# Kernel tuning notes

Measured on AMD Instinct MI355X. Metric: run time of the kernel, lower is better.

## Reference

```python
import jax, jax.numpy as jnp
import numpy as np

D_MODEL = 2048
N_HEADS = 16
HEAD_DIM = D_MODEL // N_HEADS
CLIP_QKV = 6.0
LN_EPS = 1e-5


def _layernorm(x, g, b):
    mu = jnp.mean(x, axis=-1, keepdims=True)
    var = jnp.mean(jnp.square(x - mu), axis=-1, keepdims=True)
    return (x - mu) * jax.lax.rsqrt(var + LN_EPS) * g + b


def setup_inputs() -> dict:
    key = jax.random.key(0)
    ks = jax.random.split(key, 8)
    B, S = 2, 2048
    x = jax.random.normal(ks[0], (B, S, D_MODEL), dtype=jnp.float32)
    attn_bias = jax.random.normal(ks[1], (1, N_HEADS, 1, S), dtype=jnp.float32)
    key_padding_mask = jnp.ones((B, S), dtype=bool)
    Wqkv_w = jax.random.normal(ks[2], (3 * D_MODEL, D_MODEL), dtype=jnp.float32) * 0.02
    Wqkv_b = jnp.zeros((3 * D_MODEL,), dtype=jnp.float32)
    q_ln_g = jnp.ones((D_MODEL,), dtype=jnp.float32)
    q_ln_b = jnp.zeros((D_MODEL,), dtype=jnp.float32)
    k_ln_g = jnp.ones((D_MODEL,), dtype=jnp.float32)
    k_ln_b = jnp.zeros((D_MODEL,), dtype=jnp.float32)
    out_w = jax.random.normal(ks[3], (D_MODEL, D_MODEL), dtype=jnp.float32) * 0.02
    out_b = jnp.zeros((D_MODEL,), dtype=jnp.float32)
    return {
        'x': x, 'attn_bias': attn_bias, 'key_padding_mask': key_padding_mask,
        'Wqkv_w': Wqkv_w, 'Wqkv_b': Wqkv_b,
        'q_ln_g': q_ln_g, 'q_ln_b': q_ln_b, 'k_ln_g': k_ln_g, 'k_ln_b': k_ln_b,
        'out_w': out_w, 'out_b': out_b,
    }


def reference(x, attn_bias, key_padding_mask, Wqkv_w, Wqkv_b,
              q_ln_g, q_ln_b, k_ln_g, k_ln_b, out_w, out_b):
    B, S, _ = x.shape
    # Fused QKV projection + clip
    qkv = jnp.einsum('bsd,ed->bse', x, Wqkv_w) + Wqkv_b
    qkv = jnp.clip(qkv, -CLIP_QKV, CLIP_QKV)
    q, k, v = jnp.split(qkv, 3, axis=-1)
    # QK LayerNorm over full d_model
    q = _layernorm(q, q_ln_g, q_ln_b)
    k = _layernorm(k, k_ln_g, k_ln_b)
    # [b, s, d_model] -> [b, h, s, head_dim]
    q = q.reshape(B, S, N_HEADS, HEAD_DIM).transpose(0, 2, 1, 3)
    k = k.reshape(B, S, N_HEADS, HEAD_DIM).transpose(0, 2, 1, 3)
    v = v.reshape(B, S, N_HEADS, HEAD_DIM).transpose(0, 2, 1, 3)
    scale = 1.0 / np.sqrt(HEAD_DIM).astype(np.float32)
    scores = jnp.einsum('bhqd,bhkd->bhqk', q, k) * scale  # [b, h, s, s]
    scores = scores + attn_bias
    neg_inf = jnp.array(-jnp.inf, dtype=scores.dtype)
    scores = jnp.where(key_padding_mask[:, None, None, :], scores, neg_inf)
    causal = jnp.tril(jnp.ones((S, S), dtype=bool))
    scores = jnp.where(causal[None, None, :, :], scores, neg_inf)
    probs = jax.nn.softmax(scores, axis=-1)
    ctx = jnp.einsum('bhqk,bhkd->bhqd', probs, v)
    ctx = ctx.transpose(0, 2, 1, 3).reshape(B, S, D_MODEL)
    out = jnp.einsum('bsd,ed->bse', ctx, out_w) + out_b
    return out
```

## Files before the change

kernel.cpp:

```cpp
#include <hip/hip_runtime.h>

typedef unsigned short u16;
typedef unsigned int u32;
typedef __bf16 bf16x8 __attribute__((ext_vector_type(8)));
typedef float f32x4 __attribute__((ext_vector_type(4)));

#define DEV static __device__ __forceinline__

constexpr int D_MODEL = 2048;
constexpr int N_HEADS = 16;
constexpr int HEAD_DIM = 128;
constexpr int BB = 2;
constexpr int S = 2048;
constexpr int NTOK = BB * S;
constexpr int E3 = 3 * D_MODEL;
constexpr float CLIP_QKV = 6.0f;
constexpr float LN_EPS = 1e-5f;
constexpr float NEG_BIG = -30000.0f;

DEV u16 f2bf(float f) {
    u32 u = __float_as_uint(f);
    u = (u + 0x7FFFu + ((u >> 16) & 1u)) >> 16;
    return (u16)u;
}
DEV float bf2f(u16 h) { return __uint_as_float(((u32)h) << 16); }

DEV void stage8_f32(const float* __restrict__ src, u16* __restrict__ dst) {
    const float4 f0 = *reinterpret_cast<const float4*>(src);
    const float4 f1 = *reinterpret_cast<const float4*>(src + 4);
    u16 h[8] = {f2bf(f0.x), f2bf(f0.y), f2bf(f0.z), f2bf(f0.w),
                f2bf(f1.x), f2bf(f1.y), f2bf(f1.z), f2bf(f1.w)};
    *reinterpret_cast<uint4*>(dst) = *reinterpret_cast<const uint4*>(h);
}

DEV void gload16(const u16* g, u16* l) {
    __builtin_amdgcn_global_load_lds(
        (const __attribute__((address_space(1))) void*)g,
        (__attribute__((address_space(3))) void*)l, 16, 0, 0);
}

__global__ __launch_bounds__(256)
void k_cvt(const float* __restrict__ s, u16* __restrict__ d, int n8) {
    const int i = blockIdx.x * 256 + threadIdx.x;
    if (i < n8) stage8_f32(s + (size_t)i * 8, d + (size_t)i * 8);
}

template<bool DO_CLIP, bool OUT32>
__global__ __launch_bounds__(256)
void k_gemm_bt(const u16* __restrict__ A, const u16* __restrict__ Bm,
               const float* __restrict__ bias, void* __restrict__ Cp,
               int M, int N, int K) {
    __shared__ __align__(16) u16 As[128 * 32];
    __shared__ __align__(16) u16 Bs[128 * 32];

    const int tid = threadIdx.x;
    const int lane = tid & 63, w = tid >> 6;
    const int quad = lane >> 4, l16 = lane & 15;
    const int wm = w >> 1, wn = w & 1;
    const int m0 = blockIdx.y * 128, n0 = blockIdx.x * 128;

    f32x4 acc[4][4] = {};

    for (int k0 = 0; k0 < K; k0 += 32) {
        __syncthreads();
        #pragma unroll
        for (int j = 0; j < 2; ++j) {
            const int c = w * 128 + j * 64 + lane;
            const int row = c >> 2, cc = c & 3;
            gload16(A  + (size_t)(m0 + row) * K + k0 + cc * 8, &As[c * 8]);
            gload16(Bm + (size_t)(n0 + row) * K + k0 + cc * 8, &Bs[c * 8]);
        }
        __syncthreads();

        bf16x8 af[4], bfv[4];
        #pragma unroll
        for (int mt = 0; mt < 4; ++mt)
            af[mt] = *reinterpret_cast<const bf16x8*>(&As[(wm * 64 + mt * 16 + l16) * 32 + quad * 8]);
        #pragma unroll
        for (int nt = 0; nt < 4; ++nt)
            bfv[nt] = *reinterpret_cast<const bf16x8*>(&Bs[(wn * 64 + nt * 16 + l16) * 32 + quad * 8]);
        #pragma unroll
        for (int mt = 0; mt < 4; ++mt)
            #pragma unroll
            for (int nt = 0; nt < 4; ++nt)
                acc[mt][nt] = __builtin_amdgcn_mfma_f32_16x16x32_bf16(af[mt], bfv[nt], acc[mt][nt], 0, 0, 0);
    }

    #pragma unroll
    for (int mt = 0; mt < 4; ++mt) {
        const int row = m0 + wm * 64 + mt * 16 + quad * 4;
        #pragma unroll
        for (int nt = 0; nt < 4; ++nt) {
            const int col = n0 + wn * 64 + nt * 16 + l16;
            const float bv = bias[col];
            #pragma unroll
            for (int r = 0; r < 4; ++r) {
                float v = acc[mt][nt][r] + bv;
                if (DO_CLIP) v = fminf(CLIP_QKV, fmaxf(-CLIP_QKV, v));
                if (OUT32)
                    ((float*)Cp)[(size_t)(row + r) * N + col] = v;
                else
                    ((u16*)Cp)[(size_t)(row + r) * N + col] = f2bf(v);
            }
        }
    }
}

__global__ __launch_bounds__(256)
void k_ln(const u16* __restrict__ qkvb,
          const float* __restrict__ gq, const float* __restrict__ bq,
          const float* __restrict__ gk, const float* __restrict__ bk,
          u16* __restrict__ qh, u16* __restrict__ kh) {
    __shared__ float red[8];
    const int tok = blockIdx.x;
    const int b = tok >> 11, s = tok & (S - 1);
    const int tid = threadIdx.x, lane = tid & 63, w = tid >> 6;

    #pragma unroll
    for (int part = 0; part < 2; ++part) {
        const int c0 = tid * 8;
        const u16* src = qkvb + (size_t)tok * E3 + part * D_MODEL + c0;
        u16 hx[8];
        *reinterpret_cast<uint4*>(hx) = *reinterpret_cast<const uint4*>(src);
        float x[8], sum = 0.f, sq = 0.f;
        #pragma unroll
        for (int j = 0; j < 8; ++j) { x[j] = bf2f(hx[j]); sum += x[j]; sq += x[j] * x[j]; }
        #pragma unroll
        for (int off = 1; off < 64; off <<= 1) {
            sum += __shfl_xor(sum, off, 64);
            sq  += __shfl_xor(sq,  off, 64);
        }
        __syncthreads();
        if (lane == 0) { red[w] = sum; red[4 + w] = sq; }
        __syncthreads();
        sum = red[0] + red[1] + red[2] + red[3];
        sq  = red[4] + red[5] + red[6] + red[7];
        const float mean = sum * (1.0f / D_MODEL);
        const float var  = fmaxf(sq * (1.0f / D_MODEL) - mean * mean, 0.0f);
        const float rstd = rsqrtf(var + LN_EPS);
        const float* g  = part ? gk : gq;
        const float* be = part ? bk : bq;
        u16 o[8];
        #pragma unroll
        for (int j = 0; j < 8; ++j)
            o[j] = f2bf((x[j] - mean) * rstd * g[c0 + j] + be[c0 + j]);
        const int h = c0 >> 7, d = c0 & (HEAD_DIM - 1);
        u16* dst = (part ? kh : qh) + ((size_t)((b * N_HEADS + h) * S + s)) * HEAD_DIM + d;
        *reinterpret_cast<uint4*>(dst) = *reinterpret_cast<uint4*>(o);
    }
}

__global__ __launch_bounds__(256)
void k_vtrans(const u16* __restrict__ qkvb, u16* __restrict__ vt) {
    constexpr int LDT = 136;
    __shared__ __align__(16) u16 tile[64 * LDT];
    const int blk = blockIdx.x;
    const int st = blk & 31, h = (blk >> 5) & 15, b = blk >> 9;
    const int s0 = st * 64;
    const int tid = threadIdx.x;

    #pragma unroll
    for (int i = 0; i < 4; ++i) {
        const int chunk = tid + i * 256;
        const int row = chunk >> 4, c8 = (chunk & 15) * 8;
        const u16* src = qkvb + (size_t)(b * S + s0 + row) * E3 + 2 * D_MODEL + h * HEAD_DIM + c8;
        *reinterpret_cast<uint4*>(&tile[row * LDT + c8]) = *reinterpret_cast<const uint4*>(src);
    }
    __syncthreads();
    #pragma unroll
    for (int i = 0; i < 4; ++i) {
        const int chunk = tid + i * 256;
        const int d = chunk >> 3, s8 = (chunk & 7) * 8;
        u16 o[8];
        #pragma unroll
        for (int j = 0; j < 8; ++j) o[j] = tile[(s8 + j) * LDT + d];
        u16* dst = vt + ((size_t)(b * N_HEADS + h) * HEAD_DIM + d) * S + s0 + s8;
        *reinterpret_cast<uint4*>(dst) = *reinterpret_cast<uint4*>(o);
    }
}

__global__ __launch_bounds__(256)
void k_attn(const u16* __restrict__ qh, const u16* __restrict__ kh,
            const u16* __restrict__ vt, const float* __restrict__ bias,
            u16* __restrict__ ctx) {
    constexpr int BQ = 128, BKV = 64;
    constexpr int LDK = 136;
    constexpr int LDV = 72;
    constexpr int LDP = 72;
    __shared__ __align__(16) u16 Ks[64 * LDK];
    __shared__ __align__(16) u16 Vs[128 * LDV];
    __shared__ __align__(16) u16 Ps[128 * LDP];

    const int blk = blockIdx.x;
    const int bh = blk & 31;
    const int qi = 15 - (blk >> 5);
    const int b = bh >> 4, h = bh & 15;
    const int q0 = qi * BQ;

    const int tid = threadIdx.x, lane = tid & 63, w = tid >> 6;
    const int quad = lane >> 4, l16 = lane & 15;

    const size_t bhS = (size_t)(b * N_HEADS + h) * S;
    const u16* Qt = qh + (bhS + q0) * HEAD_DIM;
    const u16* Kt = kh + bhS * HEAD_DIM;
    const u16* Vt = vt + (size_t)(b * N_HEADS + h) * HEAD_DIM * S;

    bf16x8 aq[2][4];
    #pragma unroll
    for (int mt = 0; mt < 2; ++mt)
        #pragma unroll
        for (int ks = 0; ks < 4; ++ks)
            aq[mt][ks] = *reinterpret_cast<const bf16x8*>(
                Qt + (size_t)(w * 32 + mt * 16 + l16) * HEAD_DIM + ks * 32 + quad * 8);

    f32x4 o[2][8] = {};
    float m_i[2][4], l_i[2][4];
    #pragma unroll
    for (int mt = 0; mt < 2; ++mt)
        #pragma unroll
        for (int r = 0; r < 4; ++r) { m_i[mt][r] = NEG_BIG; l_i[mt][r] = 0.f; }

    const float scale = 0.08838834764831845f;
    const int nkv = 2 * (qi + 1);

    for (int t = 0; t < nkv; ++t) {
        const int k0 = t * BKV;
        __syncthreads();
        #pragma unroll
        for (int i = 0; i < 4; ++i) {
            const int chunk = tid + i * 256;
            const int key = chunk >> 4, c8 = (chunk & 15) * 8;
            *reinterpret_cast<uint4*>(&Ks[key * LDK + c8]) =
                *reinterpret_cast<const uint4*>(Kt + (size_t)(k0 + key) * HEAD_DIM + c8);
        }
        #pragma unroll
        for (int i = 0; i < 4; ++i) {
            const int chunk = tid + i * 256;
            const int d = chunk >> 3, s8 = (chunk & 7) * 8;
            *reinterpret_cast<uint4*>(&Vs[d * LDV + s8]) =
                *reinterpret_cast<const uint4*>(Vt + (size_t)d * S + k0 + s8);
        }
        __syncthreads();

        f32x4 sc[2][4] = {};
        #pragma unroll
        for (int ks = 0; ks < 4; ++ks) {
            bf16x8 bk[4];
            #pragma unroll
            for (int nt = 0; nt < 4; ++nt)
                bk[nt] = *reinterpret_cast<const bf16x8*>(&Ks[(nt * 16 + l16) * LDK + ks * 32 + quad * 8]);
            #pragma unroll
            for (int mt = 0; mt < 2; ++mt)
                #pragma unroll
                for (int nt = 0; nt < 4; ++nt)
                    sc[mt][nt] = __builtin_amdgcn_mfma_f32_16x16x32_bf16(aq[mt][ks], bk[nt], sc[mt][nt], 0, 0, 0);
        }

        float bv[4];
        #pragma unroll
        for (int nt = 0; nt < 4; ++nt) bv[nt] = bias[h * S + k0 + nt * 16 + l16];
        const bool need_mask = (t >= 2 * qi);
        #pragma unroll
        for (int mt = 0; mt < 2; ++mt)
            #pragma unroll
            for (int nt = 0; nt < 4; ++nt) {
                const int kpos = k0 + nt * 16 + l16;
                #pragma unroll
                for (int r = 0; r < 4; ++r) {
                    float v = sc[mt][nt][r] * scale + bv[nt];
                    if (need_mask) {
                        const int qpos = q0 + w * 32 + mt * 16 + quad * 4 + r;
                        if (kpos > qpos) v = NEG_BIG;
                    }
                    sc[mt][nt][r] = v;
                }
            }

        #pragma unroll
        for (int mt = 0; mt < 2; ++mt)
            #pragma unroll
            for (int r = 0; r < 4; ++r) {
                float mx = fmaxf(fmaxf(sc[mt][0][r], sc[mt][1][r]), fmaxf(sc[mt][2][r], sc[mt][3][r]));
                mx = fmaxf(mx, __shfl_xor(mx, 1, 64));
                mx = fmaxf(mx, __shfl_xor(mx, 2, 64));
                mx = fmaxf(mx, __shfl_xor(mx, 4, 64));
                mx = fmaxf(mx, __shfl_xor(mx, 8, 64));
                const float mnew = fmaxf(m_i[mt][r], mx);
                const float alpha = __expf(m_i[mt][r] - mnew);
                float rs = 0.f;
                #pragma unroll
                for (int nt = 0; nt < 4; ++nt) {
                    const float p = __expf(sc[mt][nt][r] - mnew);
                    sc[mt][nt][r] = p;
                    rs += p;
                }
                rs += __shfl_xor(rs, 1, 64);
                rs += __shfl_xor(rs, 2, 64);
                rs += __shfl_xor(rs, 4, 64);
                rs += __shfl_xor(rs, 8, 64);
                l_i[mt][r] = l_i[mt][r] * alpha + rs;
                m_i[mt][r] = mnew;
                #pragma unroll
                for (int nt = 0; nt < 8; ++nt) o[mt][nt][r] *= alpha;
            }

        #pragma unroll
        for (int mt = 0; mt < 2; ++mt)
            #pragma unroll
            for (int nt = 0; nt < 4; ++nt)
                #pragma unroll
                for (int r = 0; r < 4; ++r)
                    Ps[(w * 32 + mt * 16 + quad * 4 + r) * LDP + nt * 16 + l16] = f2bf(sc[mt][nt][r]);

        __syncthreads();

        #pragma unroll
        for (int ks = 0; ks < 2; ++ks) {
            bf16x8 ap[2];
            #pragma unroll
            for (int mt = 0; mt < 2; ++mt)
                ap[mt] = *reinterpret_cast<const bf16x8*>(&Ps[(w * 32 + mt * 16 + l16) * LDP + ks * 32 + quad * 8]);
            #pragma unroll
            for (int nt = 0; nt < 8; ++nt) {
                const bf16x8 bvv = *reinterpret_cast<const bf16x8*>(&Vs[(nt * 16 + l16) * LDV + ks * 32 + quad * 8]);
                #pragma unroll
                for (int mt = 0; mt < 2; ++mt)
                    o[mt][nt] = __builtin_amdgcn_mfma_f32_16x16x32_bf16(ap[mt], bvv, o[mt][nt], 0, 0, 0);
            }
        }
    }

    #pragma unroll
    for (int mt = 0; mt < 2; ++mt)
        #pragma unroll
        for (int r = 0; r < 4; ++r) {
            const float inv_l = 1.0f / fmaxf(l_i[mt][r], 1e-20f);
            const int row = q0 + w * 32 + mt * 16 + quad * 4 + r;
            u16* dst = ctx + (size_t)(b * S + row) * D_MODEL + h * HEAD_DIM;
            #pragma unroll
            for (int nt = 0; nt < 8; ++nt)
                dst[nt * 16 + l16] = f2bf(o[mt][nt][r] * inv_l);
        }
}

extern "C" void kernel_launch(void* const* d_in, const int* in_sizes, int n_in,
                              void* d_out, int out_size, void* d_ws, size_t ws_size,
                              hipStream_t stream) {
    const float* x        = (const float*)d_in[0];
    const float* attn_bias= (const float*)d_in[1];
    const float* Wqkv_w   = (const float*)d_in[3];
    const float* Wqkv_b   = (const float*)d_in[4];
    const float* q_ln_g   = (const float*)d_in[5];
    const float* q_ln_b   = (const float*)d_in[6];
    const float* k_ln_g   = (const float*)d_in[7];
    const float* k_ln_b   = (const float*)d_in[8];
    const float* out_w    = (const float*)d_in[9];
    const float* out_b    = (const float*)d_in[10];

    char* ws = (char*)d_ws;
    u16* xb   = (u16*)ws; ws += (size_t)NTOK * D_MODEL * 2;
    u16* qkvb = (u16*)ws; ws += (size_t)NTOK * E3 * 2;
    u16* qhb  = (u16*)ws; ws += (size_t)NTOK * D_MODEL * 2;
    u16* khb  = (u16*)ws; ws += (size_t)NTOK * D_MODEL * 2;
    u16* vtb  = (u16*)ws; ws += (size_t)NTOK * D_MODEL * 2;
    u16* wqkvb = (u16*)d_out;
    u16* ctxb  = qkvb;
    u16* outwb = xb;

    k_cvt<<<(NTOK * D_MODEL / 8 + 255) / 256, 256, 0, stream>>>(x, xb, NTOK * D_MODEL / 8);
    k_cvt<<<(E3 * D_MODEL / 8 + 255) / 256, 256, 0, stream>>>(Wqkv_w, wqkvb, E3 * D_MODEL / 8);
    k_gemm_bt<true, false><<<dim3(E3 / 128, NTOK / 128), 256, 0, stream>>>(
        xb, wqkvb, Wqkv_b, qkvb, NTOK, E3, D_MODEL);
    k_ln<<<NTOK, 256, 0, stream>>>(qkvb, q_ln_g, q_ln_b, k_ln_g, k_ln_b, qhb, khb);
    k_vtrans<<<BB * N_HEADS * (S / 64), 256, 0, stream>>>(qkvb, vtb);
    k_attn<<<BB * N_HEADS * (S / 128), 256, 0, stream>>>(qhb, khb, vtb, attn_bias, ctxb);
    k_cvt<<<(D_MODEL * D_MODEL / 8 + 255) / 256, 256, 0, stream>>>(out_w, outwb, D_MODEL * D_MODEL / 8);
    k_gemm_bt<false, true><<<dim3(D_MODEL / 128, NTOK / 128), 256, 0, stream>>>(
        ctxb, outwb, out_b, d_out, NTOK, D_MODEL, D_MODEL);
}
```

Measured before the change: 485.2 us.

## Use 256x256-tile pipelined GEMM with XCD swizzle for the QKV projection

After: 479.3 us. No clear change (-1.2%).

```diff
diff --git a/kernel.cpp b/kernel.cpp
--- a/kernel.cpp
+++ b/kernel.cpp
@@ -104,6 +104,148 @@
             }
         }
     }
+}
+
+template<bool DO_CLIP, bool OUT32>
+__global__ __launch_bounds__(512, 2)
+void k_gemm256(const u16* __restrict__ A, const u16* __restrict__ Bm,
+               const float* __restrict__ bias, void* __restrict__ Cp,
+               int M, int N, int K) {
+    __shared__ __align__(16) u16 lds[2][2][2][256 * 32];
+
+    const int tid = threadIdx.x;
+    const int lane = tid & 63, w = tid >> 6;
+    const int quad = lane >> 4, l16 = lane & 15;
+    const int wm = w >> 2, wn = w & 3;
+
+    const int nwg = gridDim.x;
+    const int bid = blockIdx.x;
+    const int cpx = nwg >> 3;
+    const int swz = (bid & 7) * cpx + (bid >> 3);
+    const int gx = N >> 8;
+    const int bx = swz % gx, by = swz / gx;
+    const int m0 = by << 8, n0 = bx << 8;
+    const int NT = K >> 6;
+
+    u32 offA[2], offB[2];
+    int loff[2];
+    #pragma unroll
+    for (int i = 0; i < 2; ++i) {
+        const int c = i * 512 + w * 64 + lane;
+        const int row = c >> 2;
+        const int colb = ((c & 3) * 16) ^ ((row & 3) << 4);
+        offA[i] = (u32)(m0 + row) * (u32)K + (u32)(colb >> 1);
+        offB[i] = (u32)(n0 + row) * (u32)K + (u32)(colb >> 1);
+        loff[i] = c * 8;
+    }
+
+    auto STAGE = [&](int buf, int op, int kh, int kt) {
+        const u16* g = op ? Bm : A;
+        const u32* of = op ? offB : offA;
+        u16* l = lds[buf][op][kh];
+        #pragma unroll
+        for (int i = 0; i < 2; ++i)
+            gload16(g + (size_t)of[i] + (size_t)(kt + kh * 32), l + loff[i]);
+    };
+
+    bf16x8 af[4], bfr[4];
+    auto LDA = [&](int buf, int kh, int qm) {
+        const u16* base = lds[buf][0][kh];
+        #pragma unroll
+        for (int mt = 0; mt < 4; ++mt) {
+            const int row = wm * 128 + qm * 64 + mt * 16 + l16;
+            af[mt] = *reinterpret_cast<const bf16x8*>(
+                base + row * 32 + (((quad * 16) ^ ((row & 3) << 4)) >> 1));
+        }
+    };
+    auto LDB = [&](int buf, int kh) {
+        const u16* base = lds[buf][1][kh];
+        #pragma unroll
+        for (int nt = 0; nt < 4; ++nt) {
+            const int row = wn * 64 + nt * 16 + l16;
+            bfr[nt] = *reinterpret_cast<const bf16x8*>(
+                base + row * 32 + (((quad * 16) ^ ((row & 3) << 4)) >> 1));
+        }
+    };
+
+    f32x4 acc[2][4][4] = {};
+    auto MM = [&](f32x4 (&ac)[4][4]) {
+        __builtin_amdgcn_s_setprio(1);
+        #pragma unroll
+        for (int mt = 0; mt < 4; ++mt)
+            #pragma unroll
+            for (int nt = 0; nt < 4; ++nt)
+                ac[mt][nt] = __builtin_amdgcn_mfma_f32_16x16x32_bf16(
+                    af[mt], bfr[nt], ac[mt][nt], 0, 0, 0);
+        __builtin_amdgcn_s_setprio(0);
+    };
+
+    STAGE(0, 0, 0, 0); STAGE(0, 1, 0, 0); STAGE(0, 0, 1, 0); STAGE(0, 1, 1, 0);
+    if (NT > 1) {
+        STAGE(1, 1, 0, 64); STAGE(1, 0, 0, 64); STAGE(1, 1, 1, 64);
+        asm volatile("s_waitcnt vmcnt(6)" ::: "memory");
+    } else {
+        asm volatile("s_waitcnt vmcnt(0)" ::: "memory");
+    }
+    __builtin_amdgcn_s_barrier();
+    __builtin_amdgcn_sched_barrier(0);
+
+    for (int t = 0; t < NT; ++t) {
+        const int p = t & 1;
+        const int kt2 = (t + 2) << 6;
+
+        LDA(p, 0, 0); LDB(p, 0);
+        if (t + 1 < NT) STAGE(p ^ 1, 0, 1, (t + 1) << 6);
+        __builtin_amdgcn_s_barrier();
+        asm volatile("s_waitcnt lgkmcnt(0)");
+        MM(acc[0]);
+        __builtin_amdgcn_s_barrier();
+
+        LDA(p, 0, 1);
+        if (t + 2 < NT) STAGE(p, 1, 0, kt2);
+        __builtin_amdgcn_s_barrier();
+        asm volatile("s_waitcnt lgkmcnt(0)");
+        MM(acc[1]);
+        __builtin_amdgcn_s_barrier();
+
+        LDA(p, 1, 0); LDB(p, 1);
+        if (t + 2 < NT) STAGE(p, 0, 0, kt2);
+        __builtin_amdgcn_s_barrier();
+        asm volatile("s_waitcnt lgkmcnt(0)");
+        MM(acc[0]);
+        __builtin_amdgcn_s_barrier();
+
+        LDA(p, 1, 1);
+        if (t + 2 < NT) STAGE(p, 1, 1, kt2);
+        __builtin_amdgcn_s_barrier();
+        asm volatile("s_waitcnt lgkmcnt(0)");
+        MM(acc[1]);
+        if (t + 2 < NT)      asm volatile("s_waitcnt vmcnt(6)" ::: "memory");
+        else if (t + 1 < NT) asm volatile("s_waitcnt vmcnt(0)" ::: "memory");
+        __builtin_amdgcn_s_barrier();
+        __builtin_amdgcn_sched_barrier(0);
+    }
+
+    #pragma unroll
+    for (int qm = 0; qm < 2; ++qm)
+        #pragma unroll
+        for (int mt = 0; mt < 4; ++mt) {
+            const int row = m0 + wm * 128 + qm * 64 + mt * 16 + quad * 4;
+            #pragma unroll
+            for (int nt = 0; nt < 4; ++nt) {
+                const int col = n0 + wn * 64 + nt * 16 + l16;
+                const float bv = bias[col];
+                #pragma unroll
+                for (int r = 0; r < 4; ++r) {
+                    float v = acc[qm][mt][nt][r] + bv;
+                    if (DO_CLIP) v = fminf(CLIP_QKV, fmaxf(-CLIP_QKV, v));
+                    if (OUT32)
+                        ((float*)Cp)[(size_t)(row + r) * N + col] = v;
+                    else
+                        ((u16*)Cp)[(size_t)(row + r) * N + col] = f2bf(v);
+                }
+            }
+        }
 }
 
 __global__ __launch_bounds__(256)
@@ -369,7 +511,7 @@
 
     k_cvt<<<(NTOK * D_MODEL / 8 + 255) / 256, 256, 0, stream>>>(x, xb, NTOK * D_MODEL / 8);
     k_cvt<<<(E3 * D_MODEL / 8 + 255) / 256, 256, 0, stream>>>(Wqkv_w, wqkvb, E3 * D_MODEL / 8);
-    k_gemm_bt<true, false><<<dim3(E3 / 128, NTOK / 128), 256, 0, stream>>>(
+    k_gemm256<true, false><<<(E3 / 256) * (NTOK / 256), 512, 0, stream>>>(
         xb, wqkvb, Wqkv_b, qkvb, NTOK, E3, D_MODEL);
     k_ln<<<NTOK, 256, 0, stream>>>(qkvb, q_ln_g, q_ln_b, k_ln_g, k_ln_b, qhb, khb);
     k_vtrans<<<BB * N_HEADS * (S / 64), 256, 0, stream>>>(qkvb, vtb);
```
